# Kernel tuning notes

Measured on AMD Instinct MI355X. Metric: run time of the kernel, lower is better.

Reference implementation:

```python
import jax, jax.numpy as jnp
import numpy as np

WIN = 20  # rebalancing window length, hard-coded as 20 in the source


def setup_inputs() -> dict:
    key = jax.random.key(0)
    kY = jax.random.fold_in(key, 1)
    # returns-like data, small scale so covariances are well behaved
    Y = jax.random.normal(kY, (20000, 256), dtype=jnp.float32) * 0.01
    a = jnp.ones((1,), dtype=jnp.float32)
    b = jnp.ones((1,), dtype=jnp.float32)
    return {"Y": Y, "a": a, "b": b, "lag": 24}


def _ewma_gmv(Y, a, lag):
    n, p = Y.shape
    nt = lag * WIN                      # train window length = 480
    n_win = n // WIN - lag              # number of backtest windows

    starts = jnp.arange(n_win) * WIN                      # (i-lag)*20
    tr_idx = starts[:, None] + jnp.arange(nt)             # [n_win, nt]
    te_idx = (starts + nt)[:, None] + jnp.arange(WIN)
    Y_tr = Y[tr_idx]                                      # [W, nt, p]
    Y_te = Y[te_idx]

    # EWMA weights: w_t = a**(nt-1-t), normalized to sum to nt (shared by all windows)
    t = jnp.arange(nt - 1, -1, -1, dtype=Y.dtype)
    w = a[0] ** t
    w = w / w.sum() * nt                                  # [nt]

    # EWMA mean and centered data
    mean = jnp.einsum('t,wtp->wp', w, Y_tr) / nt          # [W, p]
    Yc = Y_tr - mean[:, None, :]                          # [W, nt, p]

    # EWMA sample covariance ('S' estimator):
    # Sigma = Yc^T diag(w) Yc / nt / (1 - sum(w^2)/nt^2)
    denom = nt * (1.0 - (w ** 2).sum() / (nt * nt))
    Sigma = jnp.einsum('wtp,wtq->wpq', Yc * w[None, :, None], Yc) / denom

    # GMV portfolio: w_opt = Sigma^{-1} wb / (wb^T Sigma^{-1} wb), wb = 1/p
    wb = jnp.full((p,), 1.0 / p, dtype=Y.dtype)
    x = jnp.linalg.solve(Sigma, jnp.broadcast_to(wb, (n_win, p))[..., None])[..., 0]
    w_opt = x / jnp.einsum('wp,p->w', x, wb)[:, None]     # [W, p]

    # realized test-window portfolio returns
    r = jnp.einsum('wtp,wp->wt', Y_te, w_opt)
    res_e = r.sum(axis=1)                                 # realized return over window
    res_s = jnp.var(r, axis=1, ddof=1)                    # realized daily variance

    vol = jnp.sqrt(res_s.mean() * 252.0)
    mu = res_e.mean() / WIN * 252.0
    sharpe = mu / vol
    return vol, mu, sharpe


def reference(Y, a, b, lag):
    # b only enters alpha/beta, which are unused by the 'S' estimator branch
    return _ewma_gmv(Y, a, lag)
```

## Files before the change

kernel.cpp:

```cpp
#include <hip/hip_runtime.h>
#include <math.h>

#define N_TOT   20000
#define P       256
#define WIN     20
#define LAG     24
#define NT      (LAG*WIN)
#define NB      (N_TOT/WIN)
#define NW      (NB - LAG)
#define N16T    136
#define TILEB   (N16T*256)
#define DTE     TILEB
#define NSUB4   (N16T*16)
#define ODW     (TILEB/4)
#define CG_ITERS 12

#if defined(__has_builtin)
# if __has_builtin(__builtin_amdgcn_cvt_pk_f32_fp8) && __has_builtin(__builtin_amdgcn_cvt_pk_fp8_f32)
#  define HW_FP8 1
# endif
#endif
#ifndef HW_FP8
# define HW_FP8 0
#endif

typedef float v2f   __attribute__((ext_vector_type(2)));
typedef float f32x4 __attribute__((ext_vector_type(4)));

__device__ __forceinline__ float bfr2f(unsigned short s) {
    union { unsigned int u; float f; } z; z.u = ((unsigned int)s) << 16; return z.f;
}
__device__ __forceinline__ float lo16f(unsigned int u) {
    union { unsigned int u; float f; } z; z.u = u << 16; return z.f;
}
__device__ __forceinline__ float hi16f(unsigned int u) {
    union { unsigned int u; float f; } z; z.u = u & 0xffff0000u; return z.f;
}
__device__ __forceinline__ unsigned short f2bfr(float f) {
    union { unsigned int u; float f; } z; z.f = f;
    unsigned int u = z.u;
    unsigned int r = (u + 0x7fffu + ((u >> 16) & 1u)) >> 16;
    return (unsigned short)r;
}

__device__ __forceinline__ unsigned char f2fp8(float f) {
#if HW_FP8
    int r = __builtin_amdgcn_cvt_pk_fp8_f32(f, f, 0, false);
    return (unsigned char)(r & 0xff);
#else
    union { float f; unsigned int u; } z; z.f = f;
    unsigned int s = (z.u >> 24) & 0x80u;
    float af = fabsf(f);
    if (af < 0.0009765625f) return (unsigned char)s;
    if (af >= 448.f)        return (unsigned char)(s | 0x7Eu);
    if (af < 0.015625f) {
        unsigned int m = (unsigned int)(af * 512.f + 0.5f);
        return (unsigned char)(s | m);
    }
    unsigned int au = (z.u & 0x7fffffffu) + 0x00080000u;
    unsigned int e  = (au >> 23) - 120u;
    unsigned int m  = (au >> 20) & 0x7u;
    if (e >= 16u) return (unsigned char)(s | 0x7Eu);
    return (unsigned char)(s | (e << 3) | m);
#endif
}

#if !HW_FP8
__device__ __forceinline__ float fp82f(unsigned char b) {
    unsigned int e = (b >> 3) & 0xFu;
    unsigned int m = b & 7u;
    float v;
    if (e) { union { unsigned int u; float f; } t; t.u = ((e + 120u) << 23) | (m << 20); v = t.f; }
    else   { v = (float)m * 0.001953125f; }
    return (b & 0x80u) ? -v : v;
}
#endif

__device__ __forceinline__ unsigned int pack4_fp8(float a, float b, float c, float d) {
#if HW_FP8
    int u = __builtin_amdgcn_cvt_pk_fp8_f32(a, b, 0, false);
    u = __builtin_amdgcn_cvt_pk_fp8_f32(c, d, u, true);
    return (unsigned int)u;
#else
    return (unsigned int)f2fp8(a) | ((unsigned int)f2fp8(b) << 8) |
           ((unsigned int)f2fp8(c) << 16) | ((unsigned int)f2fp8(d) << 24);
#endif
}
__device__ __forceinline__ void unpack4_fp8(unsigned int u, float* o) {
#if HW_FP8
    v2f lo = __builtin_amdgcn_cvt_pk_f32_fp8(u, false);
    v2f hi = __builtin_amdgcn_cvt_pk_f32_fp8(u, true);
    o[0] = lo.x; o[1] = lo.y; o[2] = hi.x; o[3] = hi.y;
#else
    o[0] = fp82f((unsigned char)(u & 0xff));
    o[1] = fp82f((unsigned char)((u >> 8) & 0xff));
    o[2] = fp82f((unsigned char)((u >> 16) & 0xff));
    o[3] = fp82f((unsigned char)((u >> 24) & 0xff));
#endif
}

__device__ __forceinline__ f32x4 mfma_fp8(long a, long b, f32x4 c) {
    return __builtin_amdgcn_mfma_f32_16x16x32_fp8_fp8(a, b, c, 0, 0, 0);
}

__global__ void k_init(float* acc) { acc[0] = 0.f; acc[1] = 0.f; }

__global__ void k_fallback(float* out) { out[0] = 0.f; out[1] = 0.f; out[2] = 0.f; }

__global__ __launch_bounds__(256)
void k_blocks(const float* __restrict__ Y, const float* __restrict__ pa,
              unsigned short* __restrict__ D, float* __restrict__ Dd,
              float* __restrict__ R, int base_blk)
{
    __shared__ float Ys[WIN][P];
    __shared__ float Yw[WIN][P];
    const int krel = blockIdx.x;
    const int kg   = base_blk + krel;
    const int tid  = threadIdx.x;
    const float a  = pa[0];

    float wts[WIN];
    wts[WIN-1] = 1.f;
    #pragma unroll
    for (int t = WIN-2; t >= 0; --t) wts[t] = wts[t+1] * a;

    float racc = 0.f;
    #pragma unroll
    for (int t = 0; t < WIN; ++t) {
        float v  = Y[(size_t)(kg*WIN + t)*P + tid];
        float wv = wts[t] * v;
        Ys[t][tid] = v;
        Yw[t][tid] = wv;
        racc += wv;
    }
    R[(size_t)kg*P + tid] = racc;
    __syncthreads();

    unsigned short* Dk = D + (size_t)krel * DTE;
    for (int T = tid; T < NSUB4; T += 256) {
        int t16 = T >> 4, sub = T & 15;
        int ti = (int)((sqrtf(8.f*(float)t16 + 1.f) - 1.f) * 0.5f);
        while ((ti+1)*(ti+2)/2 <= t16) ++ti;
        while (ti*(ti+1)/2 > t16) --ti;
        int tj = t16 - ti*(ti+1)/2;
        int r4 = sub >> 2, c4 = sub & 3;
        int i0 = ti*16 + r4*4, j0 = tj*16 + c4*4;

        float c[4][4] = {{0.f}};
        for (int t = 0; t < WIN; ++t) {
            float4 av = *(const float4*)&Yw[t][i0];
            float4 bv = *(const float4*)&Ys[t][j0];
            float aa[4] = {av.x, av.y, av.z, av.w};
            float bb[4] = {bv.x, bv.y, bv.z, bv.w};
            #pragma unroll
            for (int r = 0; r < 4; ++r)
                #pragma unroll
                for (int cc = 0; cc < 4; ++cc)
                    c[r][cc] = fmaf(aa[r], bb[cc], c[r][cc]);
        }
        unsigned short* tp = Dk + (size_t)t16*256 + (r4*4)*16 + c4*4;
        #pragma unroll
        for (int r = 0; r < 4; ++r) {
            unsigned int u0 = (unsigned int)f2bfr(c[r][0]) | ((unsigned int)f2bfr(c[r][1]) << 16);
            unsigned int u1 = (unsigned int)f2bfr(c[r][2]) | ((unsigned int)f2bfr(c[r][3]) << 16);
            uint2 uv; uv.x = u0; uv.y = u1;
            *(uint2*)(tp + r*16) = uv;
        }
        if (i0 == j0) {
            #pragma unroll
            for (int r = 0; r < 4; ++r)
                Dd[(size_t)krel*P + i0 + r] = c[r][r];
        }
    }
}

__global__ __launch_bounds__(256)
void k_scale(const float* __restrict__ Dd, const float* __restrict__ R,
             const float* __restrict__ pa, float* __restrict__ Sc,
             float* __restrict__ Sscale, int base_w)
{
    __shared__ float kred[4];
    const int wl  = blockIdx.x;
    const int w   = base_w + wl;
    const int i   = threadIdx.x;
    const int lane = i & 63;
    const int wid  = i >> 6;
    const float a = pa[0];

    float a20 = 1.f;
    #pragma unroll
    for (int q = 0; q < WIN; ++q) a20 *= a;
    float Wsum;
    if (fabsf(a - 1.f) < 1e-6f) Wsum = (float)NT;
    else {
        float a480 = 1.f;
        #pragma unroll
        for (int q = 0; q < LAG; ++q) a480 *= a20;
        Wsum = (a480 - 1.f) / (a - 1.f);
    }
    const float invW = 1.f / Wsum;

    float s = 0.f, sd = 0.f, tp = 1.f;
    for (int b = LAG-1; b >= 0; --b) {
        s  = fmaf(tp, R [(size_t)(w  + b)*P + i], s);
        sd = fmaf(tp, Dd[(size_t)(wl + b)*P + i], sd);
        tp *= a20;
    }
    Sc[(size_t)wl*P + i] = s * sqrtf(invW);

    float d_i = sd - s*s*invW;
    float dm = d_i;
    #pragma unroll
    for (int off = 32; off; off >>= 1) dm = fmaxf(dm, __shfl_down(dm, off));
    if (lane == 0) kred[wid] = dm;
    __syncthreads();
    if (i == 0) {
        float maxd = fmaxf(fmaxf(kred[0], kred[1]), fmaxf(kred[2], kred[3]));
        Sscale[wl] = 64.f / maxd;
    }
}

__global__ __launch_bounds__(256)
void k_conv(const unsigned short* __restrict__ D, const float* __restrict__ pa,
            const float* __restrict__ Sc, const float* __restrict__ Sscale,
            unsigned char* __restrict__ Mt, int SC_)
{
    const int od = blockIdx.x*256 + threadIdx.x;
    const int w0 = blockIdx.y * SC_;
    const float a = pa[0];

    float a20 = 1.f;
    #pragma unroll
    for (int q = 0; q < WIN; ++q) a20 *= a;
    float c23 = 1.f;
    #pragma unroll
    for (int q = 0; q < LAG-1; ++q) c23 *= a20;
    const float nc23 = -c23;

    const int t = od >> 6, q = od & 63;
    int ti = (int)((sqrtf(8.f*(float)t + 1.f) - 1.f) * 0.5f);
    while ((ti+1)*(ti+2)/2 <= t) ++ti;
    while (ti*(ti+1)/2 > t) --ti;
    const int tj = t - ti*(ti+1)/2;
    const int i  = ti*16 + (q >> 2);
    const int j0 = tj*16 + (q & 3)*4;

    const unsigned short* Dp = D + (size_t)w0*DTE + od*4;

    float m0 = 0.f, m1 = 0.f, m2 = 0.f, m3 = 0.f;
    unsigned int rg0[LAG], rg1[LAG];
    #pragma unroll
    for (int b = 0; b < LAG; ++b) {
        uint2 ev = *(const uint2*)(Dp + (size_t)b*DTE);
        rg0[b] = ev.x; rg1[b] = ev.y;
        m0 = fmaf(m0, a20, lo16f(ev.x));
        m1 = fmaf(m1, a20, hi16f(ev.x));
        m2 = fmaf(m2, a20, lo16f(ev.y));
        m3 = fmaf(m3, a20, hi16f(ev.y));
    }

    for (int sg = 0; sg < SC_; sg += LAG) {
        #pragma unroll
        for (int k = 0; k < LAG; ++k) {
            const int s = sg + k;
            if (s >= SC_) break;
            const int w = w0 + s;
            const float* scr = Sc + (size_t)w*P;
            float  sci = scr[i];
            float4 scj = *(const float4*)(scr + j0);
            float  ssc = Sscale[w];
            float c0 = fmaf(-sci, scj.x, m0) * ssc;
            float c1 = fmaf(-sci, scj.y, m1) * ssc;
            float c2 = fmaf(-sci, scj.z, m2) * ssc;
            float c3 = fmaf(-sci, scj.w, m3) * ssc;
            *(unsigned int*)(Mt + (size_t)w*TILEB + od*4) = pack4_fp8(c0, c1, c2, c3);
            uint2 ev = *(const uint2*)(Dp + (size_t)(s + LAG)*DTE);
            m0 = fmaf(fmaf(nc23, lo16f(rg0[k]), m0), a20, lo16f(ev.x));
            m1 = fmaf(fmaf(nc23, hi16f(rg0[k]), m1), a20, hi16f(ev.x));
            m2 = fmaf(fmaf(nc23, lo16f(rg1[k]), m2), a20, lo16f(ev.y));
            m3 = fmaf(fmaf(nc23, hi16f(rg1[k]), m3), a20, hi16f(ev.y));
            rg0[k] = ev.x; rg1[k] = ev.y;
        }
    }
}

__global__ __launch_bounds__(512, 4)
void k_solve(const unsigned char* __restrict__ Mt, const float* __restrict__ Y,
             float* __restrict__ acc, int base_w)
{
    __shared__ __align__(16) unsigned char Ms[TILEB];
    __shared__ __align__(16) float xs[P];
    __shared__ __align__(16) unsigned int rf8[128];
    __shared__ __align__(16) float red[16];
    __shared__ float qs[WIN];

    const int wloc = blockIdx.x;
    const int w    = base_w + wloc;
    const int tid  = threadIdx.x;
    const int lane = tid & 63;
    const int wid  = tid >> 6;
    const int g    = lane >> 4;
    const int r15  = lane & 15;
    const int g8   = g * 8;

    {
        const unsigned char* src = Mt + (size_t)wloc * TILEB;
        typedef const __attribute__((address_space(1))) unsigned int* gp1;
        typedef __attribute__((address_space(3))) unsigned int* lp3;
        for (int cb = wid; cb < 34; cb += 8) {
            __builtin_amdgcn_global_load_lds((gp1)(src + cb*1024 + lane*16),
                                             (lp3)(Ms + cb*1024), 16, 0, 0);
        }
    }
    if (tid < 64)       rf8[tid] = 0x38383838u;
    else if (tid < 128) rf8[tid] = 0u;
    __syncthreads();

    const int RTa[2] = { wid, 15 - wid };
    long afr[2][8];
    #pragma unroll
    for (int t = 0; t < 2; ++t) {
        const int rt = RTa[t];
        #pragma unroll
        for (int ks = 0; ks < 8; ++ks) {
            const int kt = ks*2 + (g >> 1);
            const int sb = (g & 1) * 8;
            long v;
            if (kt <= rt) {
                v = *(const long*)&Ms[(size_t)(rt*(rt+1)/2 + kt)*256 + r15*16 + sb];
            } else {
                const unsigned char* bp = &Ms[(size_t)(kt*(kt+1)/2 + rt)*256 + sb*16 + r15];
                unsigned int lo =  (unsigned int)bp[0]         | ((unsigned int)bp[16] << 8)
                                | ((unsigned int)bp[32] << 16) | ((unsigned int)bp[48] << 24);
                unsigned int hi =  (unsigned int)bp[64]        | ((unsigned int)bp[80] << 8)
                                | ((unsigned int)bp[96] << 16) | ((unsigned int)bp[112] << 24);
                v = (long)(((unsigned long)hi << 32) | lo);
            }
            afr[t][ks] = v;
        }
    }

    float rr[2][4], pp[2][4], ssv[2][4], xx[2][4];
    #pragma unroll
    for (int t = 0; t < 2; ++t)
        #pragma unroll
        for (int r = 0; r < 4; ++r) { rr[t][r] = 1.f; pp[t][r] = 0.f; ssv[t][r] = 0.f; xx[t][r] = 0.f; }

    const unsigned char* rfb = (const unsigned char*)rf8;
    float mu_p = 1.f, alpha_p = 1.f;
    for (int it = 0; it < CG_ITERS; ++it) {
        f32x4 ah0 = {0.f,0.f,0.f,0.f}, ah1 = {0.f,0.f,0.f,0.f};
        f32x4 al0 = {0.f,0.f,0.f,0.f}, al1 = {0.f,0.f,0.f,0.f};
        #pragma unroll
        for (int ks = 0; ks < 8; ++ks) {
            long bh = *(const long*)(rfb + ks*32 + g8);
            long bl = *(const long*)(rfb + 256 + ks*32 + g8);
            ah0 = mfma_fp8(afr[0][ks], bh, ah0);
            ah1 = mfma_fp8(afr[1][ks], bh, ah1);
            al0 = mfma_fp8(afr[0][ks], bl, al0);
            al1 = mfma_fp8(afr[1][ks], bl, al1);
        }
        float w0[4], w1[4];
        #pragma unroll
        for (int r = 0; r < 4; ++r) {
            w0[r] = fmaf(al0[r], 0.0625f, ah0[r]);
            w1[r] = fmaf(al1[r], 0.0625f, ah1[r]);
        }

        float mu_c = 0.f, nu_c = 0.f;
        #pragma unroll
        for (int r = 0; r < 4; ++r) {
            mu_c += rr[0][r]*rr[0][r] + rr[1][r]*rr[1][r];
            nu_c  = fmaf(rr[0][r], w0[r], nu_c);
            nu_c  = fmaf(rr[1][r], w1[r], nu_c);
        }
        if (r15 != 0) { mu_c = 0.f; nu_c = 0.f; }
        mu_c += __shfl_down(mu_c, 32); nu_c += __shfl_down(nu_c, 32);
        mu_c += __shfl_down(mu_c, 16); nu_c += __shfl_down(nu_c, 16);
        if (lane == 0) { red[wid] = mu_c; red[8 + wid] = nu_c; }
        __syncthreads();
        float mu = red[0]+red[1]+red[2]+red[3]+red[4]+red[5]+red[6]+red[7];
        float nu = red[8]+red[9]+red[10]+red[11]+red[12]+red[13]+red[14]+red[15];

        float beta  = (it == 0) ? 0.f : mu / mu_p;
        float alpha = (it == 0) ? mu / nu
                                : mu / (nu - beta * mu / alpha_p);
        mu_p = mu; alpha_p = alpha;

        #pragma unroll
        for (int t = 0; t < 2; ++t)
            #pragma unroll
            for (int r = 0; r < 4; ++r) {
                float wv = t ? w1[r] : w0[r];
                pp[t][r]  = fmaf(beta, pp[t][r], rr[t][r]);
                ssv[t][r] = fmaf(beta, ssv[t][r], wv);
                xx[t][r]  = fmaf(alpha, pp[t][r], xx[t][r]);
                rr[t][r]  = fmaf(-alpha, ssv[t][r], rr[t][r]);
            }

        if (r15 == 0 && it != CG_ITERS-1) {
            #pragma unroll
            for (int t = 0; t < 2; ++t) {
                unsigned int hv = pack4_fp8(rr[t][0], rr[t][1], rr[t][2], rr[t][3]);
                float dec[4];
                unpack4_fp8(hv, dec);
                unsigned int lv = pack4_fp8((rr[t][0]-dec[0])*16.f, (rr[t][1]-dec[1])*16.f,
                                            (rr[t][2]-dec[2])*16.f, (rr[t][3]-dec[3])*16.f);
                int idx = RTa[t]*4 + g;
                rf8[idx]      = hv;
                rf8[64 + idx] = lv;
            }
        }
        __syncthreads();
    }

    if (r15 == 0) {
        #pragma unroll
        for (int t = 0; t < 2; ++t)
            *(float4*)&xs[RTa[t]*16 + g*4] =
                make_float4(xx[t][0], xx[t][1], xx[t][2], xx[t][3]);
    }
    float sv = 0.f;
    #pragma unroll
    for (int t = 0; t < 2; ++t)
        #pragma unroll
        for (int r = 0; r < 4; ++r) sv += xx[t][r];
    if (r15 != 0) sv = 0.f;
    sv += __shfl_down(sv, 32); sv += __shfl_down(sv, 16);
    if (lane == 0) red[wid] = sv;
    __syncthreads();
    float sumx = red[0]+red[1]+red[2]+red[3]+red[4]+red[5]+red[6]+red[7];

    const float* Yte = Y + (size_t)(w*WIN + NT) * P;
    for (int t = wid; t < WIN; t += 8) {
        float4 yv = *(const float4*)&Yte[(size_t)t*P + lane*4];
        float4 xv = *(const float4*)&xs[lane*4];
        float q = yv.x*xv.x + yv.y*xv.y + yv.z*xv.z + yv.w*xv.w;
        #pragma unroll
        for (int off = 32; off; off >>= 1) q += __shfl_down(q, off);
        if (lane == 0) qs[t] = q;
    }
    __syncthreads();

    if (tid == 0) {
        float scl = (float)P / sumx;
        float rsv[WIN];
        float re = 0.f;
        #pragma unroll
        for (int t = 0; t < WIN; ++t) { rsv[t] = qs[t]*scl; re += rsv[t]; }
        float mean = re / (float)WIN;
        float var = 0.f;
        #pragma unroll
        for (int t = 0; t < WIN; ++t) { float d = rsv[t] - mean; var = fmaf(d, d, var); }
        var /= (float)(WIN - 1);
        atomicAdd(&acc[0], re);
        atomicAdd(&acc[1], var);
    }
}

__global__ void k_final(const float* __restrict__ acc, float* __restrict__ out)
{
    float mean_s = acc[1] / (float)NW;
    float vol = sqrtf(mean_s * 252.f);
    float mu  = (acc[0] / (float)NW) / (float)WIN * 252.f;
    out[0] = vol;
    out[1] = mu;
    out[2] = mu / vol;
}

static inline size_t align_up(size_t x) { return (x + 255) & ~(size_t)255; }

extern "C" void kernel_launch(void* const* d_in, const int* in_sizes, int n_in,
                              void* d_out, int out_size, void* d_ws, size_t ws_size,
                              hipStream_t stream)
{
    const float* Y  = (const float*)d_in[0];
    const float* pa = (const float*)d_in[1];
    float* out = (float*)d_out;

    static const int nch_opts[] = {1, 2, 4, 8, 16, 61};
    int CW = -1;
    size_t oDd = 0, oMt = 0, oR = 0, oSc = 0, oSs = 0, oAcc = 0;
    for (int oi = 0; oi < 6; ++oi) {
        int cw = NW / nch_opts[oi];
        size_t dB  = align_up((size_t)(cw + LAG) * DTE * 2);
        size_t ddB = align_up((size_t)(cw + LAG) * P * 4);
        size_t mB  = align_up((size_t)cw * TILEB);
        size_t rB  = align_up((size_t)NB * P * 4);
        size_t scB = align_up((size_t)cw * P * 4);
        size_t ssB = align_up((size_t)cw * 4);
        size_t tot = dB + ddB + mB + rB + scB + ssB + 256;
        if (tot <= ws_size) {
            CW = cw; oDd = dB; oMt = dB + ddB; oR = oMt + mB;
            oSc = oR + rB; oSs = oSc + scB; oAcc = oSs + ssB;
            break;
        }
    }
    if (CW < 0) {
        hipLaunchKernelGGL(k_fallback, dim3(1), dim3(1), 0, stream, out);
        return;
    }
    const int NCH  = NW / CW;
    const int SC   = (CW % 61 == 0) ? 61 : CW;
    const int NSUB = CW / SC;

    char* ws = (char*)d_ws;
    unsigned short* D   = (unsigned short*)(ws);
    float*          Dd  = (float*)(ws + oDd);
    unsigned char*  Mt  = (unsigned char*)(ws + oMt);
    float*          R   = (float*)(ws + oR);
    float*          Sc  = (float*)(ws + oSc);
    float*          Ssc = (float*)(ws + oSs);
    float*          acc = (float*)(ws + oAcc);

    hipLaunchKernelGGL(k_init, dim3(1), dim3(1), 0, stream, acc);
    for (int c = 0; c < NCH; ++c) {
        const int base_w = c * CW;
        hipLaunchKernelGGL(k_blocks, dim3(CW + LAG),      dim3(256), 0, stream,
                           Y, pa, D, Dd, R, base_w);
        hipLaunchKernelGGL(k_scale,  dim3(CW),            dim3(256), 0, stream,
                           Dd, R, pa, Sc, Ssc, base_w);
        hipLaunchKernelGGL(k_conv,   dim3(ODW/256, NSUB), dim3(256), 0, stream,
                           D, pa, Sc, Ssc, Mt, SC);
        hipLaunchKernelGGL(k_solve,  dim3(CW),            dim3(512), 0, stream,
                           Mt, Y, acc, base_w);
    }
    hipLaunchKernelGGL(k_final, dim3(1), dim3(1), 0, stream, acc, out);
}
```

Baseline: 198.6 us.

## Run CG solve with a single wavefront per window, keeping the matrix in registers

The k_solve kernel now uses one 64-thread wavefront per window instead of eight waves. Each lane holds all 16 row tiles of the fp8 covariance in registers (128 longs), so the block-wide barriers for the dot-product reductions become wave-level xor shuffles. The transposed-tile byte gather is rewritten to read 32-bit words and extract bytes instead of issuing single-byte LDS loads. The MFMA output is staged through shared memory and redistributed so each lane owns 4 vector entries. The cost is very high register pressure and 8x less parallelism per block, since each wave issues all MFMAs serially. Occupancy drops and spilling is a risk.

Result: slower. 211.4 us (+6.4%).

```diff
diff --git a/kernel.cpp b/kernel.cpp
--- a/kernel.cpp
+++ b/kernel.cpp
@@ -284,43 +284,36 @@
     }
 }
 
-__global__ __launch_bounds__(512, 4)
+__global__ __launch_bounds__(64, 1)
 void k_solve(const unsigned char* __restrict__ Mt, const float* __restrict__ Y,
              float* __restrict__ acc, int base_w)
 {
     __shared__ __align__(16) unsigned char Ms[TILEB];
-    __shared__ __align__(16) float xs[P];
+    __shared__ __align__(16) float ws2[2][P];
     __shared__ __align__(16) unsigned int rf8[128];
-    __shared__ __align__(16) float red[16];
-    __shared__ float qs[WIN];
 
     const int wloc = blockIdx.x;
     const int w    = base_w + wloc;
-    const int tid  = threadIdx.x;
-    const int lane = tid & 63;
-    const int wid  = tid >> 6;
+    const int lane = threadIdx.x;
     const int g    = lane >> 4;
     const int r15  = lane & 15;
-    const int g8   = g * 8;
 
     {
         const unsigned char* src = Mt + (size_t)wloc * TILEB;
         typedef const __attribute__((address_space(1))) unsigned int* gp1;
         typedef __attribute__((address_space(3))) unsigned int* lp3;
-        for (int cb = wid; cb < 34; cb += 8) {
+        for (int cb = 0; cb < 34; ++cb) {
             __builtin_amdgcn_global_load_lds((gp1)(src + cb*1024 + lane*16),
                                              (lp3)(Ms + cb*1024), 16, 0, 0);
         }
     }
-    if (tid < 64)       rf8[tid] = 0x38383838u;
-    else if (tid < 128) rf8[tid] = 0u;
+    rf8[lane]      = 0x38383838u;
+    rf8[64 + lane] = 0u;
     __syncthreads();
 
-    const int RTa[2] = { wid, 15 - wid };
-    long afr[2][8];
-    #pragma unroll
-    for (int t = 0; t < 2; ++t) {
-        const int rt = RTa[t];
+    long afr[16][8];
+    #pragma unroll
+    for (int rt = 0; rt < 16; ++rt) {
         #pragma unroll
         for (int ks = 0; ks < 8; ++ks) {
             const int kt = ks*2 + (g >> 1);
@@ -329,129 +322,124 @@
             if (kt <= rt) {
                 v = *(const long*)&Ms[(size_t)(rt*(rt+1)/2 + kt)*256 + r15*16 + sb];
             } else {
-                const unsigned char* bp = &Ms[(size_t)(kt*(kt+1)/2 + rt)*256 + sb*16 + r15];
-                unsigned int lo =  (unsigned int)bp[0]         | ((unsigned int)bp[16] << 8)
-                                | ((unsigned int)bp[32] << 16) | ((unsigned int)bp[48] << 24);
-                unsigned int hi =  (unsigned int)bp[64]        | ((unsigned int)bp[80] << 8)
-                                | ((unsigned int)bp[96] << 16) | ((unsigned int)bp[112] << 24);
-                v = (long)(((unsigned long)hi << 32) | lo);
+                const unsigned char* tp2 =
+                    &Ms[(size_t)(kt*(kt+1)/2 + rt)*256 + sb*16 + (r15 & ~3)];
+                const int sh = (r15 & 3) * 8;
+                unsigned int b0 = 0, b1 = 0;
+                #pragma unroll
+                for (int q2 = 0; q2 < 4; ++q2) {
+                    unsigned int d0 = *(const unsigned int*)(tp2 + q2*16);
+                    unsigned int d1 = *(const unsigned int*)(tp2 + (q2+4)*16);
+                    b0 |= ((d0 >> sh) & 0xffu) << (q2*8);
+                    b1 |= ((d1 >> sh) & 0xffu) << (q2*8);
+                }
+                v = (long)(((unsigned long)b1 << 32) | b0);
             }
-            afr[t][ks] = v;
-        }
-    }
-
-    float rr[2][4], pp[2][4], ssv[2][4], xx[2][4];
-    #pragma unroll
-    for (int t = 0; t < 2; ++t)
-        #pragma unroll
-        for (int r = 0; r < 4; ++r) { rr[t][r] = 1.f; pp[t][r] = 0.f; ssv[t][r] = 0.f; xx[t][r] = 0.f; }
-
-    const unsigned char* rfb = (const unsigned char*)rf8;
+            afr[rt][ks] = v;
+        }
+    }
+
+    float rr[4], pp[4], sv[4], xx[4];
+    #pragma unroll
+    for (int j = 0; j < 4; ++j) { rr[j] = 1.f; pp[j] = 0.f; sv[j] = 0.f; xx[j] = 0.f; }
+
+    const int widx = ((lane >> 1) & 3)*16 + (lane >> 3)*2 + (lane & 1);
+    const char* rfb = (const char*)rf8;
+
     float mu_p = 1.f, alpha_p = 1.f;
     for (int it = 0; it < CG_ITERS; ++it) {
-        f32x4 ah0 = {0.f,0.f,0.f,0.f}, ah1 = {0.f,0.f,0.f,0.f};
-        f32x4 al0 = {0.f,0.f,0.f,0.f}, al1 = {0.f,0.f,0.f,0.f};
-        #pragma unroll
-        for (int ks = 0; ks < 8; ++ks) {
-            long bh = *(const long*)(rfb + ks*32 + g8);
-            long bl = *(const long*)(rfb + 256 + ks*32 + g8);
-            ah0 = mfma_fp8(afr[0][ks], bh, ah0);
-            ah1 = mfma_fp8(afr[1][ks], bh, ah1);
-            al0 = mfma_fp8(afr[0][ks], bl, al0);
-            al1 = mfma_fp8(afr[1][ks], bl, al1);
-        }
-        float w0[4], w1[4];
-        #pragma unroll
-        for (int r = 0; r < 4; ++r) {
-            w0[r] = fmaf(al0[r], 0.0625f, ah0[r]);
-            w1[r] = fmaf(al1[r], 0.0625f, ah1[r]);
-        }
-
-        float mu_c = 0.f, nu_c = 0.f;
-        #pragma unroll
-        for (int r = 0; r < 4; ++r) {
-            mu_c += rr[0][r]*rr[0][r] + rr[1][r]*rr[1][r];
-            nu_c  = fmaf(rr[0][r], w0[r], nu_c);
-            nu_c  = fmaf(rr[1][r], w1[r], nu_c);
-        }
-        if (r15 != 0) { mu_c = 0.f; nu_c = 0.f; }
-        mu_c += __shfl_down(mu_c, 32); nu_c += __shfl_down(nu_c, 32);
-        mu_c += __shfl_down(mu_c, 16); nu_c += __shfl_down(nu_c, 16);
-        if (lane == 0) { red[wid] = mu_c; red[8 + wid] = nu_c; }
+        long bq[8];
+        #pragma unroll
+        for (int kp = 0; kp < 4; ++kp) {
+            long2 bv; bv.x = 0; bv.y = 0;
+            if (r15 < 2) bv = *(const long2*)(rfb + (r15 << 8) + (g << 6) + (kp << 4));
+            bq[2*kp]   = bv.x;
+            bq[2*kp+1] = bv.y;
+        }
+        #pragma unroll
+        for (int rt = 0; rt < 16; ++rt) {
+            f32x4 a4 = {0.f, 0.f, 0.f, 0.f};
+            #pragma unroll
+            for (int ks = 0; ks < 8; ++ks)
+                a4 = mfma_fp8(afr[rt][ks], bq[ks], a4);
+            if (r15 < 2) {
+                float4 o; o.x = a4[0]; o.y = a4[1]; o.z = a4[2]; o.w = a4[3];
+                *(float4*)&ws2[r15][rt*16 + g*4] = o;
+            }
+        }
         __syncthreads();
-        float mu = red[0]+red[1]+red[2]+red[3]+red[4]+red[5]+red[6]+red[7];
-        float nu = red[8]+red[9]+red[10]+red[11]+red[12]+red[13]+red[14]+red[15];
-
-        float beta  = (it == 0) ? 0.f : mu / mu_p;
-        float alpha = (it == 0) ? mu / nu
-                                : mu / (nu - beta * mu / alpha_p);
-        mu_p = mu; alpha_p = alpha;
-
-        #pragma unroll
-        for (int t = 0; t < 2; ++t)
-            #pragma unroll
-            for (int r = 0; r < 4; ++r) {
-                float wv = t ? w1[r] : w0[r];
-                pp[t][r]  = fmaf(beta, pp[t][r], rr[t][r]);
-                ssv[t][r] = fmaf(beta, ssv[t][r], wv);
-                xx[t][r]  = fmaf(alpha, pp[t][r], xx[t][r]);
-                rr[t][r]  = fmaf(-alpha, ssv[t][r], rr[t][r]);
-            }
-
-        if (r15 == 0 && it != CG_ITERS-1) {
-            #pragma unroll
-            for (int t = 0; t < 2; ++t) {
-                unsigned int hv = pack4_fp8(rr[t][0], rr[t][1], rr[t][2], rr[t][3]);
-                float dec[4];
-                unpack4_fp8(hv, dec);
-                unsigned int lv = pack4_fp8((rr[t][0]-dec[0])*16.f, (rr[t][1]-dec[1])*16.f,
-                                            (rr[t][2]-dec[2])*16.f, (rr[t][3]-dec[3])*16.f);
-                int idx = RTa[t]*4 + g;
-                rf8[idx]      = hv;
-                rf8[64 + idx] = lv;
-            }
+
+        float4 hi4 = *(const float4*)&ws2[0][lane*4];
+        float4 lo4 = *(const float4*)&ws2[1][lane*4];
+        float w4[4] = { fmaf(lo4.x, 0.0625f, hi4.x), fmaf(lo4.y, 0.0625f, hi4.y),
+                        fmaf(lo4.z, 0.0625f, hi4.z), fmaf(lo4.w, 0.0625f, hi4.w) };
+
+        float mu_c = rr[0]*rr[0] + rr[1]*rr[1] + rr[2]*rr[2] + rr[3]*rr[3];
+        float nu_c = rr[0]*w4[0];
+        nu_c = fmaf(rr[1], w4[1], nu_c);
+        nu_c = fmaf(rr[2], w4[2], nu_c);
+        nu_c = fmaf(rr[3], w4[3], nu_c);
+        #pragma unroll
+        for (int off = 1; off < 64; off <<= 1) {
+            mu_c += __shfl_xor(mu_c, off);
+            nu_c += __shfl_xor(nu_c, off);
+        }
+
+        float beta  = (it == 0) ? 0.f : mu_c / mu_p;
+        float alpha = (it == 0) ? mu_c / nu_c
+                                : mu_c / (nu_c - beta * mu_c / alpha_p);
+        mu_p = mu_c; alpha_p = alpha;
+
+        #pragma unroll
+        for (int j = 0; j < 4; ++j) {
+            pp[j] = fmaf(beta,  pp[j], rr[j]);
+            sv[j] = fmaf(beta,  sv[j], w4[j]);
+            xx[j] = fmaf(alpha, pp[j], xx[j]);
+            rr[j] = fmaf(-alpha, sv[j], rr[j]);
+        }
+
+        if (it != CG_ITERS-1) {
+            unsigned int hv = pack4_fp8(rr[0], rr[1], rr[2], rr[3]);
+            float dec[4];
+            unpack4_fp8(hv, dec);
+            unsigned int lv = pack4_fp8((rr[0]-dec[0])*16.f, (rr[1]-dec[1])*16.f,
+                                        (rr[2]-dec[2])*16.f, (rr[3]-dec[3])*16.f);
+            rf8[widx]      = hv;
+            rf8[64 + widx] = lv;
         }
         __syncthreads();
     }
 
-    if (r15 == 0) {
-        #pragma unroll
-        for (int t = 0; t < 2; ++t)
-            *(float4*)&xs[RTa[t]*16 + g*4] =
-                make_float4(xx[t][0], xx[t][1], xx[t][2], xx[t][3]);
-    }
-    float sv = 0.f;
-    #pragma unroll
-    for (int t = 0; t < 2; ++t)
-        #pragma unroll
-        for (int r = 0; r < 4; ++r) sv += xx[t][r];
-    if (r15 != 0) sv = 0.f;
-    sv += __shfl_down(sv, 32); sv += __shfl_down(sv, 16);
-    if (lane == 0) red[wid] = sv;
-    __syncthreads();
-    float sumx = red[0]+red[1]+red[2]+red[3]+red[4]+red[5]+red[6]+red[7];
+    float sumx = xx[0] + xx[1] + xx[2] + xx[3];
+    #pragma unroll
+    for (int off = 1; off < 64; off <<= 1) sumx += __shfl_xor(sumx, off);
 
     const float* Yte = Y + (size_t)(w*WIN + NT) * P;
-    for (int t = wid; t < WIN; t += 8) {
+    float qv[WIN];
+    #pragma unroll
+    for (int t = 0; t < WIN; ++t) {
         float4 yv = *(const float4*)&Yte[(size_t)t*P + lane*4];
-        float4 xv = *(const float4*)&xs[lane*4];
-        float q = yv.x*xv.x + yv.y*xv.y + yv.z*xv.z + yv.w*xv.w;
-        #pragma unroll
-        for (int off = 32; off; off >>= 1) q += __shfl_down(q, off);
-        if (lane == 0) qs[t] = q;
-    }
-    __syncthreads();
-
-    if (tid == 0) {
+        float q = yv.x*xx[0];
+        q = fmaf(yv.y, xx[1], q);
+        q = fmaf(yv.z, xx[2], q);
+        q = fmaf(yv.w, xx[3], q);
+        qv[t] = q;
+    }
+    #pragma unroll
+    for (int off = 1; off < 64; off <<= 1) {
+        #pragma unroll
+        for (int t = 0; t < WIN; ++t) qv[t] += __shfl_xor(qv[t], off);
+    }
+
+    if (lane == 0) {
         float scl = (float)P / sumx;
-        float rsv[WIN];
         float re = 0.f;
         #pragma unroll
-        for (int t = 0; t < WIN; ++t) { rsv[t] = qs[t]*scl; re += rsv[t]; }
+        for (int t = 0; t < WIN; ++t) { qv[t] *= scl; re += qv[t]; }
         float mean = re / (float)WIN;
         float var = 0.f;
         #pragma unroll
-        for (int t = 0; t < WIN; ++t) { float d = rsv[t] - mean; var = fmaf(d, d, var); }
+        for (int t = 0; t < WIN; ++t) { float d = qv[t] - mean; var = fmaf(d, d, var); }
         var /= (float)(WIN - 1);
         atomicAdd(&acc[0], re);
         atomicAdd(&acc[1], var);
@@ -522,7 +510,7 @@
                            Dd, R, pa, Sc, Ssc, base_w);
         hipLaunchKernelGGL(k_conv,   dim3(ODW/256, NSUB), dim3(256), 0, stream,
                            D, pa, Sc, Ssc, Mt, SC);
-        hipLaunchKernelGGL(k_solve,  dim3(CW),            dim3(512), 0, stream,
+        hipLaunchKernelGGL(k_solve,  dim3(CW),            dim3(64),  0, stream,
                            Mt, Y, acc, base_w);
     }
     hipLaunchKernelGGL(k_final, dim3(1), dim3(1), 0, stream, acc, out);
```
